# Optimization experiments

Measured on AMD Instinct MI355X. Metric: run time of the kernel, lower is better.

The kernel has to match this reference:

```python
import jax, jax.numpy as jnp
import numpy as np

EMB_DIM = 768
QKV_DIM = 64
NUM_HEAD = 12


def setup_inputs() -> dict:
    key = jax.random.key(0)
    k1, k2, k3 = jax.random.split(key, 3)
    z = jax.random.normal(k1, (16, 1024, EMB_DIM), dtype=jnp.float32)
    U_qkv = jax.random.normal(k2, (NUM_HEAD, 3, EMB_DIM, QKV_DIM), dtype=jnp.float32) * (1.0 / np.sqrt(EMB_DIM))
    U_msa = jax.random.normal(k3, (NUM_HEAD * QKV_DIM, EMB_DIM), dtype=jnp.float32) * (1.0 / np.sqrt(NUM_HEAD * QKV_DIM))
    return {"z": z, "U_qkv": U_qkv, "U_msa": U_msa}


def reference(z, U_qkv, U_msa):
    # z: [b, n, e]; U_qkv: [h, 3, e, d]; U_msa: [h*d, e]
    qkv = jnp.einsum("bne,hked->khbnd", z, U_qkv)  # [3, h, b, n, d]
    q, k, v = qkv[0], qkv[1], qkv[2]               # each [h, b, n, d]
    scale = 1.0 / jnp.sqrt(jnp.asarray(q.shape[-1], dtype=z.dtype))
    logits = jnp.einsum("hbnd,hbmd->hbnm", q, k) * scale  # [h, b, n, n]
    attn = jax.nn.softmax(logits, axis=-1)
    o = jnp.einsum("hbnm,hbmd->bnhd", attn, v)     # [b, n, h, d]
    b, n = o.shape[0], o.shape[1]
    o = o.reshape(b, n, -1)                        # [b, n, h*d]
    return o @ U_msa                               # [b, n, e]
```

## Files before the change

kernel.cpp:

```cpp
#include <hip/hip_runtime.h>
#include <hip/hip_bf16.h>

typedef _Float16 f16x8 __attribute__((ext_vector_type(8)));
typedef _Float16 f16x4 __attribute__((ext_vector_type(4)));
typedef float f32x4 __attribute__((ext_vector_type(4)));

#define MFMA32(a, b, c) __builtin_amdgcn_mfma_f32_16x16x32_f16(a, b, c, 0, 0, 0)
#define MFMA16(a, b, c) __builtin_amdgcn_mfma_f32_16x16x16f16(a, b, c, 0, 0, 0)

__global__ __launch_bounds__(256) void tconv_kernel(
    const float* __restrict__ in, _Float16* __restrict__ out, int R, int C) {
  size_t bat = (size_t)blockIdx.y * R * C;
  int o = blockIdx.x * 256 + threadIdx.x;
  if (o < R * C) {
    int c = o / R, r = o - c * R;
    out[bat + o] = (_Float16)in[bat + (size_t)r * C + c];
  }
}

__global__ __launch_bounds__(256) void cvt16_kernel(
    const float* __restrict__ in, _Float16* __restrict__ out, int n) {
  int i = (blockIdx.x * 256 + threadIdx.x) * 8;
  if (i < n) {
    float4 a = *(const float4*)(in + i);
    float4 b = *(const float4*)(in + i + 4);
    f16x8 cv;
    cv[0] = (_Float16)a.x; cv[1] = (_Float16)a.y;
    cv[2] = (_Float16)a.z; cv[3] = (_Float16)a.w;
    cv[4] = (_Float16)b.x; cv[5] = (_Float16)b.y;
    cv[6] = (_Float16)b.z; cv[7] = (_Float16)b.w;
    *(f16x8*)(out + i) = cv;
  }
}

__global__ __launch_bounds__(256) void qkv_gemm_kernel(
    const _Float16* __restrict__ zh, const _Float16* __restrict__ Ut,
    _Float16* __restrict__ Qf, _Float16* __restrict__ Kf,
    _Float16* __restrict__ Vt) {
  __shared__ _Float16 As[128][72];
  __shared__ _Float16 Bs[128][72];

  const int tid = threadIdx.x;
  const int wv = tid >> 6, lane = tid & 63, quad = lane >> 4, l16 = lane & 15;
  const int m0 = blockIdx.x * 128;
  const int n0 = blockIdx.y * 128;

  f32x4 acc[2][8] = {};

  for (int k0 = 0; k0 < 768; k0 += 64) {
    __syncthreads();
#pragma unroll
    for (int i = 0; i < 4; ++i) {
      int ch = i * 256 + tid;
      int r = ch >> 3, cc = (ch & 7) << 3;
      *(uint4*)&As[r][cc] =
          *(const uint4*)(zh + (size_t)(m0 + r) * 768 + k0 + cc);
      *(uint4*)&Bs[r][cc] =
          *(const uint4*)(Ut + (size_t)(n0 + r) * 768 + k0 + cc);
    }
    __syncthreads();
#pragma unroll
    for (int ks = 0; ks < 2; ++ks) {
      f16x8 af[2], bfr[8];
#pragma unroll
      for (int rt = 0; rt < 2; ++rt)
        af[rt] = *(const f16x8*)&As[wv * 32 + rt * 16 + l16][ks * 32 + quad * 8];
#pragma unroll
      for (int ct = 0; ct < 8; ++ct)
        bfr[ct] = *(const f16x8*)&Bs[ct * 16 + l16][ks * 32 + quad * 8];
#pragma unroll
      for (int rt = 0; rt < 2; ++rt)
#pragma unroll
        for (int ct = 0; ct < 8; ++ct)
          acc[rt][ct] = MFMA32(af[rt], bfr[ct], acc[rt][ct]);
    }
  }

#pragma unroll
  for (int ct = 0; ct < 8; ++ct) {
    const int g = blockIdx.y * 2 + (ct >> 2);
    const int h = g / 3, kk = g - h * 3;
    const int dd = (ct & 3) * 16 + l16;
#pragma unroll
    for (int rt = 0; rt < 2; ++rt) {
#pragma unroll
      for (int r = 0; r < 4; ++r) {
        int m = m0 + wv * 32 + rt * 16 + quad * 4 + r;
        int b = m >> 10, n = m & 1023;
        _Float16 val = (_Float16)acc[rt][ct][r];
        if (kk == 0)
          Qf[(((size_t)h * 16 + b) * 1024 + n) * 64 + dd] = val;
        else if (kk == 1)
          Kf[(((size_t)h * 16 + b) * 1024 + n) * 64 + dd] = val;
        else
          Vt[(((size_t)h * 16 + b) * 64 + dd) * 1024 + n] = val;
      }
    }
  }
}

__global__ __launch_bounds__(256) void attn_kernel(
    const _Float16* __restrict__ Qf, const _Float16* __restrict__ Kf,
    const _Float16* __restrict__ Vt, _Float16* __restrict__ Of) {
  __shared__ _Float16 Ks[64][72];
  __shared__ _Float16 Vs[64][72];

  const int tid = threadIdx.x;
  const int wv = tid >> 6, lane = tid & 63, quad = lane >> 4, l16 = lane & 15;
  const int hb = blockIdx.x;
  const int h = hb >> 4, b = hb & 15;
  const _Float16* Q = Qf + (size_t)hb * 65536;
  const _Float16* K = Kf + (size_t)hb * 65536;
  const _Float16* V = Vt + (size_t)hb * 65536;
  const int q0 = blockIdx.y * 128 + wv * 32;

  const _Float16 cs = (_Float16)0.18033688011112042f;
  f16x8 qfr[2][2];
#pragma unroll
  for (int mi = 0; mi < 2; ++mi) {
    const _Float16* qp = Q + (size_t)(q0 + mi * 16 + l16) * 64 + quad * 8;
    qfr[mi][0] = *(const f16x8*)qp * cs;
    qfr[mi][1] = *(const f16x8*)(qp + 32) * cs;
  }

  const int r0 = tid >> 3, c0 = (tid & 7) << 3;
  const _Float16* Kst = K + (size_t)r0 * 64 + c0;
  const _Float16* Vst = V + (size_t)r0 * 1024 + c0;

  uint4 kreg[2], vreg[2];
#pragma unroll
  for (int i = 0; i < 2; ++i) {
    kreg[i] = *(const uint4*)(Kst + i * 2048);
    vreg[i] = *(const uint4*)(Vst + i * 32768);
  }

  f32x4 o[2][4] = {};
  float lsum[2] = {};

  for (int t = 0; t < 16; ++t) {
#pragma unroll
    for (int i = 0; i < 2; ++i) {
      *(uint4*)&Ks[r0 + i * 32][c0] = kreg[i];
      *(uint4*)&Vs[r0 + i * 32][c0] = vreg[i];
    }
    __syncthreads();
    if (t < 15) {
      int n1 = (t + 1) * 64;
#pragma unroll
      for (int i = 0; i < 2; ++i) {
        kreg[i] = *(const uint4*)(Kst + (size_t)n1 * 64 + i * 2048);
        vreg[i] = *(const uint4*)(Vst + n1 + i * 32768);
      }
    }

    f32x4 st[2][4] = {};
#pragma unroll
    for (int ct = 0; ct < 4; ++ct) {
      f16x8 k0 = *(const f16x8*)&Ks[ct * 16 + l16][quad * 8];
      f16x8 k1 = *(const f16x8*)&Ks[ct * 16 + l16][32 + quad * 8];
#pragma unroll
      for (int mi = 0; mi < 2; ++mi) {
        st[mi][ct] = MFMA32(k0, qfr[mi][0], st[mi][ct]);
        st[mi][ct] = MFMA32(k1, qfr[mi][1], st[mi][ct]);
      }
    }

    f16x4 pa[2][4];
#pragma unroll
    for (int mi = 0; mi < 2; ++mi)
#pragma unroll
      for (int ct = 0; ct < 4; ++ct)
#pragma unroll
        for (int r = 0; r < 4; ++r) {
          float p = __builtin_amdgcn_exp2f(st[mi][ct][r]);
          lsum[mi] += p;
          pa[mi][ct][r] = (_Float16)p;
        }

#pragma unroll
    for (int dt = 0; dt < 4; ++dt) {
#pragma unroll
      for (int kb = 0; kb < 4; ++kb) {
        f16x4 vf = *(const f16x4*)&Vs[dt * 16 + l16][kb * 16 + quad * 4];
#pragma unroll
        for (int mi = 0; mi < 2; ++mi)
          o[mi][dt] = MFMA16(pa[mi][kb], vf, o[mi][dt]);
      }
    }
    __syncthreads();
  }

#pragma unroll
  for (int mi = 0; mi < 2; ++mi) {
    float s = lsum[mi];
    s += __shfl_xor(s, 16, 64);
    s += __shfl_xor(s, 32, 64);
    lsum[mi] = s;
  }

#pragma unroll
  for (int mi = 0; mi < 2; ++mi) {
#pragma unroll
    for (int r = 0; r < 4; ++r) {
      float inv = 1.f / __shfl(lsum[mi], quad * 4 + r, 64);
      int n = q0 + mi * 16 + quad * 4 + r;
#pragma unroll
      for (int dt = 0; dt < 4; ++dt) {
        int dd = dt * 16 + l16;
        Of[((size_t)b * 1024 + n) * 768 + h * 64 + dd] =
            (_Float16)(o[mi][dt][r] * inv);
      }
    }
  }
}

__global__ __launch_bounds__(256) void out_gemm_kernel(
    const _Float16* __restrict__ A, const _Float16* __restrict__ Bt,
    float* __restrict__ Cout) {
  __shared__ _Float16 As[128][72];
  __shared__ _Float16 Bs[128][72];

  const int tid = threadIdx.x;
  const int wv = tid >> 6, lane = tid & 63, quad = lane >> 4, l16 = lane & 15;
  const int m0 = blockIdx.x * 128;
  const int n0 = blockIdx.y * 128;

  f32x4 acc[2][8] = {};

  for (int k0 = 0; k0 < 768; k0 += 64) {
    __syncthreads();
#pragma unroll
    for (int i = 0; i < 4; ++i) {
      int ch = i * 256 + tid;
      int r = ch >> 3, cc = (ch & 7) << 3;
      *(uint4*)&As[r][cc] =
          *(const uint4*)(A + (size_t)(m0 + r) * 768 + k0 + cc);
      *(uint4*)&Bs[r][cc] =
          *(const uint4*)(Bt + (size_t)(n0 + r) * 768 + k0 + cc);
    }
    __syncthreads();
#pragma unroll
    for (int ks = 0; ks < 2; ++ks) {
      f16x8 af[2], bfr[8];
#pragma unroll
      for (int rt = 0; rt < 2; ++rt)
        af[rt] = *(const f16x8*)&As[wv * 32 + rt * 16 + l16][ks * 32 + quad * 8];
#pragma unroll
      for (int ct = 0; ct < 8; ++ct)
        bfr[ct] = *(const f16x8*)&Bs[ct * 16 + l16][ks * 32 + quad * 8];
#pragma unroll
      for (int rt = 0; rt < 2; ++rt)
#pragma unroll
        for (int ct = 0; ct < 8; ++ct)
          acc[rt][ct] = MFMA32(af[rt], bfr[ct], acc[rt][ct]);
    }
  }

#pragma unroll
  for (int rt = 0; rt < 2; ++rt) {
#pragma unroll
    for (int ct = 0; ct < 8; ++ct) {
#pragma unroll
      for (int r = 0; r < 4; ++r) {
        int m = m0 + wv * 32 + rt * 16 + quad * 4 + r;
        int n = n0 + ct * 16 + l16;
        Cout[(size_t)m * 768 + n] = acc[rt][ct][r];
      }
    }
  }
}

extern "C" void kernel_launch(void* const* d_in, const int* in_sizes, int n_in,
                              void* d_out, int out_size, void* d_ws,
                              size_t ws_size, hipStream_t stream) {
  const float* z = (const float*)d_in[0];
  const float* Uqkv = (const float*)d_in[1];
  const float* Umsa = (const float*)d_in[2];

  char* ws = (char*)d_ws;
  _Float16* Ut_qkv = (_Float16*)(ws);
  _Float16* Ut_msa = (_Float16*)(ws + 3538944);
  _Float16* zh = (_Float16*)(ws + 4718592);
  _Float16* Of = zh;
  _Float16* Qf = (_Float16*)(ws + 29884416);
  _Float16* Kf = (_Float16*)(ws + 55050240);
  _Float16* Vt = (_Float16*)(ws + 80216064);

  tconv_kernel<<<dim3(192, 36), 256, 0, stream>>>(Uqkv, Ut_qkv, 768, 64);
  tconv_kernel<<<dim3(2304, 1), 256, 0, stream>>>(Umsa, Ut_msa, 768, 768);
  cvt16_kernel<<<dim3(6144, 1), 256, 0, stream>>>(z, zh, 16384 * 768);

  qkv_gemm_kernel<<<dim3(128, 18), 256, 0, stream>>>(zh, Ut_qkv, Qf, Kf, Vt);
  attn_kernel<<<dim3(192, 8), 256, 0, stream>>>(Qf, Kf, Vt, Of);
  out_gemm_kernel<<<dim3(128, 6), 256, 0, stream>>>(Of, Ut_msa,
                                                    (float*)d_out);
}
```

Measured before the change: 391.7 us.

## Use direct global-to-LDS loads with XOR swizzle, XCD block remapping, nontemporal stores

```diff
diff --git a/kernel.cpp b/kernel.cpp
--- a/kernel.cpp
+++ b/kernel.cpp
@@ -7,6 +7,11 @@
 
 #define MFMA32(a, b, c) __builtin_amdgcn_mfma_f32_16x16x32_f16(a, b, c, 0, 0, 0)
 #define MFMA16(a, b, c) __builtin_amdgcn_mfma_f32_16x16x16f16(a, b, c, 0, 0, 0)
+
+#define GLOAD_LDS16(g, l)                                         \
+  __builtin_amdgcn_global_load_lds(                               \
+      (const __attribute__((address_space(1))) void*)(g),         \
+      (__attribute__((address_space(3))) void*)(l), 16, 0, 0)
 
 __global__ __launch_bounds__(256) void tconv_kernel(
     const float* __restrict__ in, _Float16* __restrict__ out, int R, int C) {
@@ -37,13 +42,24 @@
     const _Float16* __restrict__ zh, const _Float16* __restrict__ Ut,
     _Float16* __restrict__ Qf, _Float16* __restrict__ Kf,
     _Float16* __restrict__ Vt) {
-  __shared__ _Float16 As[128][72];
-  __shared__ _Float16 Bs[128][72];
+  __shared__ _Float16 As[128 * 64];
+  __shared__ _Float16 Bs[128 * 64];
 
   const int tid = threadIdx.x;
   const int wv = tid >> 6, lane = tid & 63, quad = lane >> 4, l16 = lane & 15;
-  const int m0 = blockIdx.x * 128;
-  const int n0 = blockIdx.y * 128;
+
+  const int flat = blockIdx.y * 128 + blockIdx.x;
+  const int swz = (flat & 7) * 288 + (flat >> 3);
+  const int m0 = (swz & 127) * 128;
+  const int by = swz >> 7;
+  const int n0 = by * 128;
+
+  const int srow = lane >> 3;
+  const int scol = ((lane & 7) ^ srow) << 3;
+  const _Float16* Ag = zh + (size_t)(m0 + srow) * 768 + scol;
+  const _Float16* Bg = Ut + (size_t)(n0 + srow) * 768 + scol;
+
+  const int cbq = quad * 16;
 
   f32x4 acc[2][8] = {};
 
@@ -51,23 +67,26 @@
     __syncthreads();
 #pragma unroll
     for (int i = 0; i < 4; ++i) {
-      int ch = i * 256 + tid;
-      int r = ch >> 3, cc = (ch & 7) << 3;
-      *(uint4*)&As[r][cc] =
-          *(const uint4*)(zh + (size_t)(m0 + r) * 768 + k0 + cc);
-      *(uint4*)&Bs[r][cc] =
-          *(const uint4*)(Ut + (size_t)(n0 + r) * 768 + k0 + cc);
+      const int rb = (i * 4 + wv) * 8;
+      GLOAD_LDS16(Ag + (size_t)rb * 768 + k0, (char*)As + rb * 128);
+      GLOAD_LDS16(Bg + (size_t)rb * 768 + k0, (char*)Bs + rb * 128);
     }
     __syncthreads();
 #pragma unroll
     for (int ks = 0; ks < 2; ++ks) {
       f16x8 af[2], bfr[8];
 #pragma unroll
-      for (int rt = 0; rt < 2; ++rt)
-        af[rt] = *(const f16x8*)&As[wv * 32 + rt * 16 + l16][ks * 32 + quad * 8];
-#pragma unroll
-      for (int ct = 0; ct < 8; ++ct)
-        bfr[ct] = *(const f16x8*)&Bs[ct * 16 + l16][ks * 32 + quad * 8];
+      for (int rt = 0; rt < 2; ++rt) {
+        const int r = wv * 32 + rt * 16 + l16;
+        af[rt] = *(const f16x8*)((const char*)As + r * 128 +
+                                 ((ks * 64 + cbq) ^ ((r & 7) << 4)));
+      }
+#pragma unroll
+      for (int ct = 0; ct < 8; ++ct) {
+        const int r = ct * 16 + l16;
+        bfr[ct] = *(const f16x8*)((const char*)Bs + r * 128 +
+                                  ((ks * 64 + cbq) ^ ((r & 7) << 4)));
+      }
 #pragma unroll
       for (int rt = 0; rt < 2; ++rt)
 #pragma unroll
@@ -78,7 +97,7 @@
 
 #pragma unroll
   for (int ct = 0; ct < 8; ++ct) {
-    const int g = blockIdx.y * 2 + (ct >> 2);
+    const int g = by * 2 + (ct >> 2);
     const int h = g / 3, kk = g - h * 3;
     const int dd = (ct & 3) * 16 + l16;
 #pragma unroll
@@ -107,12 +126,15 @@
 
   const int tid = threadIdx.x;
   const int wv = tid >> 6, lane = tid & 63, quad = lane >> 4, l16 = lane & 15;
-  const int hb = blockIdx.x;
+
+  const int flat = blockIdx.x;
+  const int swz = (flat & 7) * 192 + (flat >> 3);
+  const int hb = swz >> 3;
   const int h = hb >> 4, b = hb & 15;
   const _Float16* Q = Qf + (size_t)hb * 65536;
   const _Float16* K = Kf + (size_t)hb * 65536;
   const _Float16* V = Vt + (size_t)hb * 65536;
-  const int q0 = blockIdx.y * 128 + wv * 32;
+  const int q0 = (swz & 7) * 128 + wv * 32;
 
   const _Float16 cs = (_Float16)0.18033688011112042f;
   f16x8 qfr[2][2];
@@ -207,8 +229,9 @@
 #pragma unroll
       for (int dt = 0; dt < 4; ++dt) {
         int dd = dt * 16 + l16;
-        Of[((size_t)b * 1024 + n) * 768 + h * 64 + dd] =
-            (_Float16)(o[mi][dt][r] * inv);
+        __builtin_nontemporal_store(
+            (_Float16)(o[mi][dt][r] * inv),
+            &Of[((size_t)b * 1024 + n) * 768 + h * 64 + dd]);
       }
     }
   }
@@ -217,13 +240,23 @@
 __global__ __launch_bounds__(256) void out_gemm_kernel(
     const _Float16* __restrict__ A, const _Float16* __restrict__ Bt,
     float* __restrict__ Cout) {
-  __shared__ _Float16 As[128][72];
-  __shared__ _Float16 Bs[128][72];
+  __shared__ _Float16 As[128 * 64];
+  __shared__ _Float16 Bs[128 * 64];
 
   const int tid = threadIdx.x;
   const int wv = tid >> 6, lane = tid & 63, quad = lane >> 4, l16 = lane & 15;
-  const int m0 = blockIdx.x * 128;
-  const int n0 = blockIdx.y * 128;
+
+  const int flat = blockIdx.y * 128 + blockIdx.x;
+  const int swz = (flat & 7) * 96 + (flat >> 3);
+  const int m0 = (swz & 127) * 128;
+  const int n0 = (swz >> 7) * 128;
+
+  const int srow = lane >> 3;
+  const int scol = ((lane & 7) ^ srow) << 3;
+  const _Float16* Ag = A + (size_t)(m0 + srow) * 768 + scol;
+  const _Float16* Bg = Bt + (size_t)(n0 + srow) * 768 + scol;
+
+  const int cbq = quad * 16;
 
   f32x4 acc[2][8] = {};
 
@@ -231,23 +264,26 @@
     __syncthreads();
 #pragma unroll
     for (int i = 0; i < 4; ++i) {
-      int ch = i * 256 + tid;
-      int r = ch >> 3, cc = (ch & 7) << 3;
-      *(uint4*)&As[r][cc] =
-          *(const uint4*)(A + (size_t)(m0 + r) * 768 + k0 + cc);
-      *(uint4*)&Bs[r][cc] =
-          *(const uint4*)(Bt + (size_t)(n0 + r) * 768 + k0 + cc);
+      const int rb = (i * 4 + wv) * 8;
+      GLOAD_LDS16(Ag + (size_t)rb * 768 + k0, (char*)As + rb * 128);
+      GLOAD_LDS16(Bg + (size_t)rb * 768 + k0, (char*)Bs + rb * 128);
     }
     __syncthreads();
 #pragma unroll
     for (int ks = 0; ks < 2; ++ks) {
       f16x8 af[2], bfr[8];
 #pragma unroll
-      for (int rt = 0; rt < 2; ++rt)
-        af[rt] = *(const f16x8*)&As[wv * 32 + rt * 16 + l16][ks * 32 + quad * 8];
-#pragma unroll
-      for (int ct = 0; ct < 8; ++ct)
-        bfr[ct] = *(const f16x8*)&Bs[ct * 16 + l16][ks * 32 + quad * 8];
+      for (int rt = 0; rt < 2; ++rt) {
+        const int r = wv * 32 + rt * 16 + l16;
+        af[rt] = *(const f16x8*)((const char*)As + r * 128 +
+                                 ((ks * 64 + cbq) ^ ((r & 7) << 4)));
+      }
+#pragma unroll
+      for (int ct = 0; ct < 8; ++ct) {
+        const int r = ct * 16 + l16;
+        bfr[ct] = *(const f16x8*)((const char*)Bs + r * 128 +
+                                  ((ks * 64 + cbq) ^ ((r & 7) << 4)));
+      }
 #pragma unroll
       for (int rt = 0; rt < 2; ++rt)
 #pragma unroll
@@ -264,7 +300,8 @@
       for (int r = 0; r < 4; ++r) {
         int m = m0 + wv * 32 + rt * 16 + quad * 4 + r;
         int n = n0 + ct * 16 + l16;
-        Cout[(size_t)m * 768 + n] = acc[rt][ct][r];
+        __builtin_nontemporal_store(acc[rt][ct][r],
+                                    &Cout[(size_t)m * 768 + n]);
       }
     }
   }
@@ -291,7 +328,7 @@
   cvt16_kernel<<<dim3(6144, 1), 256, 0, stream>>>(z, zh, 16384 * 768);
 
   qkv_gemm_kernel<<<dim3(128, 18), 256, 0, stream>>>(zh, Ut_qkv, Qf, Kf, Vt);
-  attn_kernel<<<dim3(192, 8), 256, 0, stream>>>(Qf, Kf, Vt, Of);
+  attn_kernel<<<dim3(1536, 1), 256, 0, stream>>>(Qf, Kf, Vt, Of);
   out_gemm_kernel<<<dim3(128, 6), 256, 0, stream>>>(Of, Ut_msa,
                                                     (float*)d_out);
 }
```

Measured after the change: 401.1 us. 2.4% more time.
